# Kernel tuning notes

Hardware: AMD Instinct MI355X
Metric: run time of the kernel (lower is better)

Reference implementation:

```python
import jax, jax.numpy as jnp
import numpy as np

# Config constants (from CantorFusionConfigV2 defaults / init_kwargs)
NUM_HEADS = 8
HEAD_DIM = 64
K_NEIGHBORS = 64        # fusion_window
LEVELS = 5              # k_simplex + 1
TAU = 0.25
BASE = 3.0
ALPHA = 0.5
EPS = 1e-8
RESIDUAL_SCALE = 1.0


def _cantor_measure(S):
    """Vectorized Devil's Staircase Cantor measure for S positions in [0,1]. Returns [S]."""
    pos = (jnp.arange(S, dtype=jnp.float32) + 0.5) / S
    pos = jnp.clip(pos, 1e-10, 1.0 - 1e-10)
    ks = jnp.arange(1, LEVELS + 1, dtype=jnp.float32)
    scales = BASE ** ks                      # [L]
    lvl_w = 0.5 ** ks                        # [L]
    centers = jnp.array([0.5, 1.5, 2.5], dtype=jnp.float32)
    y = jnp.mod(pos[:, None] * scales, BASE)            # [S, L]
    logits = -((y[..., None] - centers) ** 2) / (TAU + 1e-10)  # [S, L, 3]
    p = jax.nn.softmax(logits, axis=-1)
    bits = p[..., 2] + ALPHA * p[..., 1]                # [S, L]
    return jnp.sum(bits * lvl_w, axis=-1)               # [S]


def _routes_and_weights(S):
    """KNN routes [S,K] by Cantor distance + inverse-distance softmax weights [S,K]."""
    cm = _cantor_measure(S)
    Dm = jnp.abs(cm[:, None] - cm[None, :])             # [S, S]
    Dm = Dm / (Dm.max() + 1e-10)
    neg_d, routes = jax.lax.top_k(-Dm, K_NEIGHBORS)     # k smallest distances
    route_dist = -neg_d                                  # [S, K]
    w = jax.nn.softmax(1.0 / (route_dist + EPS), axis=-1)
    return routes, w


def setup_inputs() -> dict:
    key = jax.random.key(0)
    k1, k2, k3 = jax.random.split(key, 3)
    B, S, D = 2, 2048, 512
    x = jax.random.normal(k1, (B, S, D), dtype=jnp.float32)
    W_in = jax.random.normal(k2, (D, D), dtype=jnp.float32) * (1.0 / np.sqrt(D))
    b_in = jnp.zeros((D,), dtype=jnp.float32)
    W_out = jax.random.normal(k3, (D, D), dtype=jnp.float32) * (1.0 / np.sqrt(D))
    b_out = jnp.zeros((D,), dtype=jnp.float32)
    return {"x": x, "W_in": W_in, "b_in": b_in, "W_out": W_out, "b_out": b_out}


def reference(x, W_in, b_in, W_out, b_out):
    B, S, dim = x.shape
    routes, w = _routes_and_weights(S)                   # [S,K], [S,K] (no-grad geometry)
    routes = jax.lax.stop_gradient(routes)
    w = jax.lax.stop_gradient(w)
    # input projection and head split -> [B, H, S, D]
    h = (x @ W_in + b_in).reshape(B, S, NUM_HEADS, HEAD_DIM).transpose(0, 2, 1, 3)
    # neighbor gather [B, H, S, K, D] then inverse-distance weighted sum
    gathered = h[:, :, routes, :]                        # [B,H,S,K,D]
    fused = jnp.einsum('bhskd,sk->bhsd', gathered, w)    # [B,H,S,D]
    out = fused.transpose(0, 2, 1, 3).reshape(B, S, dim) @ W_out + b_out
    return x + RESIDUAL_SCALE * out
```

## Files before the change

kernel.cpp:

```cpp
#include <hip/hip_runtime.h>
#include <hip/hip_bf16.h>

#define S_LEN 2048
#define K_NB  64

typedef __attribute__((ext_vector_type(8))) short bf16x8;
typedef __attribute__((ext_vector_type(4))) float f32x4;
typedef __attribute__((ext_vector_type(4))) unsigned int u32x4;

__device__ inline unsigned short f2b(float f) {
    unsigned u = __builtin_bit_cast(unsigned, f);
    return (unsigned short)((u + 0x7FFFu + ((u >> 16) & 1u)) >> 16);
}

__global__ __launch_bounds__(256) void prep_kernel(const float* __restrict__ W_in,
                                                   const float* __restrict__ W_out,
                                                   unsigned short* __restrict__ Wt_in,
                                                   unsigned short* __restrict__ Wt_out,
                                                   float* __restrict__ cmf) {
    int b = blockIdx.x;
    if (b < 256) {
        int t = b * 256 + threadIdx.x;
        const float* W = (t & 32768) ? W_out : W_in;
        unsigned short* Wt = (t & 32768) ? Wt_out : Wt_in;
        int u = t & 32767;
        int n = u & 511, kc = (u >> 9) * 8;
        unsigned short tmp[8];
        #pragma unroll
        for (int j = 0; j < 8; ++j) tmp[j] = f2b(W[(size_t)(kc + j) * 512 + n]);
        *(u32x4*)(Wt + (size_t)n * 512 + kc) = *(u32x4*)tmp;
    } else {
        int s = (b - 256) * 256 + threadIdx.x;
        float pos = ((float)s + 0.5f) * (1.0f / 2048.0f);
        float cm = 0.0f, scale = 1.0f, lvlw = 1.0f;
        #pragma unroll
        for (int k = 1; k <= 5; ++k) {
            scale *= 3.0f; lvlw *= 0.5f;
            float y = fmodf(pos * scale, 3.0f);
            float d0 = y - 0.5f, d1 = y - 1.5f, d2 = y - 2.5f;
            float l0 = -(d0 * d0) * 4.0f;
            float l1 = -(d1 * d1) * 4.0f;
            float l2 = -(d2 * d2) * 4.0f;
            float m = fmaxf(l0, fmaxf(l1, l2));
            float e0 = (float)exp((double)(l0 - m));
            float e1 = (float)exp((double)(l1 - m));
            float e2 = (float)exp((double)(l2 - m));
            float sum = (e0 + e1) + e2;
            float p1 = e1 / sum, p2 = e2 / sum;
            cm += (p2 + 0.5f * p1) * lvlw;
        }
        cmf[s] = cm;
    }
}

__global__ __launch_bounds__(64) void group_kernel(const float* __restrict__ cmf,
                                                   int* __restrict__ routes,
                                                   int* __restrict__ counts) {
    int s = blockIdx.x;
    int lane = threadIdx.x;
    float v = cmf[s];
    int n = 0;
    int* rt = routes + s * K_NB;
    for (int j0 = 0; j0 < S_LEN; j0 += 64) {
        float c = cmf[j0 + lane];
        bool m = (c == v);
        unsigned long long mask = __ballot(m);
        if (m) {
            int idx = n + __popcll(mask & ((1ull << lane) - 1ull));
            if (idx < K_NB) rt[idx] = j0 + lane;
        }
        n += __popcll(mask);
    }
    if (lane == 0) counts[s] = n < K_NB ? n : K_NB;
}

template <int EPI>
__global__ __launch_bounds__(256) void gemm_mfma(
    const float* __restrict__ Af, const unsigned short* __restrict__ Ab,
    const unsigned short* __restrict__ Bt, const float* __restrict__ bias,
    const float* __restrict__ X, unsigned short* __restrict__ Hb,
    float* __restrict__ Out,
    const int* __restrict__ routes, const int* __restrict__ counts) {
    __shared__ char lds[(64 + 128) * 64 * 2];
    char* As = lds;
    char* Bs = lds + 64 * 64 * 2;
    const int tid = threadIdx.x;
    const int bn = blockIdx.x, bm = blockIdx.y;
    const int wid = tid >> 6, lane = tid & 63;
    const int wr = wid >> 1, wc = wid & 1;
    const int l15 = lane & 15, l4 = lane >> 4;

    const int arow = tid >> 2;
    const int akq  = (tid & 3) * 16;
    const int brow = tid >> 1;
    const int bkh  = (tid & 1) * 32;

    auto off = [](int row, int k) -> int {
        int o = row * 128 + k * 2;
        return o ^ ((row & 7) << 4);
    };

    const int grow = bm * 64 + arow;
    const float* arow_f = nullptr;
    int gn = 1; const int* grt = nullptr; float ginv = 1.0f; size_t hbase = 0;
    if (EPI == 0) {
        arow_f = Af + (size_t)grow * 512;
    } else {
        int gs = grow & (S_LEN - 1), gb = grow >> 11;
        gn = counts[gs];
        grt = routes + gs * K_NB;
        ginv = 1.0f / (float)gn;
        hbase = (size_t)gb * S_LEN * 512;
    }
    const unsigned short* bsrc = Bt + (size_t)(bn * 128 + brow) * 512 + bkh;

    u32x4 arg[2] = {};
    u32x4 brg[4] = {};

    auto load_a = [&](int k0, u32x4* dst) {
        if (EPI == 0) {
            const float* p = arow_f + k0 + akq;
            unsigned short tmp[16];
            #pragma unroll
            for (int i = 0; i < 4; ++i) {
                float4 v = *(const float4*)(p + i * 4);
                tmp[i*4+0] = f2b(v.x); tmp[i*4+1] = f2b(v.y);
                tmp[i*4+2] = f2b(v.z); tmp[i*4+3] = f2b(v.w);
            }
            dst[0] = *(u32x4*)&tmp[0];
            dst[1] = *(u32x4*)&tmp[8];
        } else if (gn == 1) {
            const unsigned short* p = Ab + (size_t)grow * 512 + k0 + akq;
            dst[0] = *(const u32x4*)(p);
            dst[1] = *(const u32x4*)(p + 8);
        } else {
            float av[16] = {};
            for (int e = 0; e < gn; ++e) {
                const unsigned short* p = Ab + hbase + (size_t)grt[e] * 512 + k0 + akq;
                #pragma unroll
                for (int half = 0; half < 2; ++half) {
                    u32x4 u = *(const u32x4*)(p + half * 8);
                    #pragma unroll
                    for (int q = 0; q < 4; ++q) {
                        unsigned w = u[q];
                        av[half*8 + q*2 + 0] += __builtin_bit_cast(float, w << 16);
                        av[half*8 + q*2 + 1] += __builtin_bit_cast(float, w & 0xFFFF0000u);
                    }
                }
            }
            unsigned short tmp[16];
            #pragma unroll
            for (int i = 0; i < 16; ++i) tmp[i] = f2b(av[i] * ginv);
            dst[0] = *(u32x4*)&tmp[0];
            dst[1] = *(u32x4*)&tmp[8];
        }
    };
    auto load_b = [&](int k0, u32x4* dst) {
        const unsigned short* p = bsrc + k0;
        #pragma unroll
        for (int i = 0; i < 4; ++i) dst[i] = *(const u32x4*)(p + i * 8);
    };

    f32x4 acc[2][4] = {};

    load_a(0, arg);
    load_b(0, brg);
    for (int k0 = 0; k0 < 512; k0 += 64) {
        *(u32x4*)(As + off(arow, akq))     = arg[0];
        *(u32x4*)(As + off(arow, akq + 8)) = arg[1];
        #pragma unroll
        for (int i = 0; i < 4; ++i)
            *(u32x4*)(Bs + off(brow, bkh + i * 8)) = brg[i];
        __syncthreads();
        if (k0 + 64 < 512) {
            load_a(k0 + 64, arg);
            load_b(k0 + 64, brg);
        }
        #pragma unroll
        for (int kk = 0; kk < 2; ++kk) {
            const int kb = kk * 32 + l4 * 8;
            bf16x8 af[2], bg[4];
            #pragma unroll
            for (int m = 0; m < 2; ++m)
                af[m] = *(bf16x8*)(As + off(wr * 32 + m * 16 + l15, kb));
            #pragma unroll
            for (int n = 0; n < 4; ++n)
                bg[n] = *(bf16x8*)(Bs + off(wc * 64 + n * 16 + l15, kb));
            #pragma unroll
            for (int m = 0; m < 2; ++m)
                #pragma unroll
                for (int n = 0; n < 4; ++n)
                    acc[m][n] = __builtin_amdgcn_mfma_f32_16x16x32_bf16(
                        af[m], bg[n], acc[m][n], 0, 0, 0);
        }
        __syncthreads();
    }

    float bv[4];
    #pragma unroll
    for (int n = 0; n < 4; ++n) bv[n] = bias[bn * 128 + wc * 64 + n * 16 + l15];
    #pragma unroll
    for (int m = 0; m < 2; ++m) {
        #pragma unroll
        for (int r = 0; r < 4; ++r) {
            int row = bm * 64 + wr * 32 + m * 16 + l4 * 4 + r;
            #pragma unroll
            for (int n = 0; n < 4; ++n) {
                int col = bn * 128 + wc * 64 + n * 16 + l15;
                float v = acc[m][n][r] + bv[n];
                if (EPI == 0)
                    Hb[(size_t)row * 512 + col] = f2b(v);
                else
                    Out[(size_t)row * 512 + col] = X[(size_t)row * 512 + col] + v;
            }
        }
    }
}

extern "C" void kernel_launch(void* const* d_in, const int* in_sizes, int n_in,
                              void* d_out, int out_size, void* d_ws, size_t ws_size,
                              hipStream_t stream) {
    const float* x     = (const float*)d_in[0];
    const float* W_in  = (const float*)d_in[1];
    const float* b_in  = (const float*)d_in[2];
    const float* W_out = (const float*)d_in[3];
    const float* b_out = (const float*)d_in[4];
    float* out = (float*)d_out;

    char* ws = (char*)d_ws;
    float*          cmf    = (float*)ws;
    int*            counts = (int*)(ws + 8192);
    int*            routes = (int*)(ws + 16384);
    unsigned short* Wt_in  = (unsigned short*)(ws + 16384 + 524288);
    unsigned short* Wt_out = (unsigned short*)(ws + 16384 + 2 * 524288);
    unsigned short* h      = (unsigned short*)(ws + 16384 + 3 * 524288);

    prep_kernel<<<264, 256, 0, stream>>>(W_in, W_out, Wt_in, Wt_out, cmf);
    group_kernel<<<S_LEN, 64, 0, stream>>>(cmf, routes, counts);
    gemm_mfma<0><<<dim3(4, 64), 256, 0, stream>>>(x, nullptr, Wt_in, b_in,
                                                  nullptr, h, nullptr,
                                                  nullptr, nullptr);
    gemm_mfma<1><<<dim3(4, 64), 256, 0, stream>>>(nullptr, h, Wt_out, b_out,
                                                  x, nullptr, out,
                                                  routes, counts);
}
```

Measured before the change: 36.57 us.

## Fold both projections into one combined weight and gather from x directly

Because the gather-average is linear, the two projections are folded into one combined weight (W_in·W_out) and a combined bias (b_in·W_out + b_out). A small MFMA GEMM computes the combined weight, and it runs in the same launch as the grouping step. The final GEMM then gathers and averages rows of x instead of a precomputed h, which removes the full 4096x512x512 input-projection GEMM and one kernel launch. In exchange, the combined weight is rounded to bf16 and the gather now reads fp32 x rows, which changes numerics slightly.

```diff
diff --git a/kernel.cpp b/kernel.cpp
--- a/kernel.cpp
+++ b/kernel.cpp
@@ -13,24 +13,33 @@
     return (unsigned short)((u + 0x7FFFu + ((u >> 16) & 1u)) >> 16);
 }
 
-__global__ __launch_bounds__(256) void prep_kernel(const float* __restrict__ W_in,
-                                                   const float* __restrict__ W_out,
-                                                   unsigned short* __restrict__ Wt_in,
-                                                   unsigned short* __restrict__ Wt_out,
-                                                   float* __restrict__ cmf) {
-    int b = blockIdx.x;
-    if (b < 256) {
-        int t = b * 256 + threadIdx.x;
-        const float* W = (t & 32768) ? W_out : W_in;
-        unsigned short* Wt = (t & 32768) ? Wt_out : Wt_in;
-        int u = t & 32767;
+__device__ inline int swoff(int row, int k) {
+    int o = row * 128 + k * 2;
+    return o ^ ((row & 7) << 4);
+}
+
+__global__ __launch_bounds__(256) void prep_kernel(
+    const float* __restrict__ W_in, const float* __restrict__ W_out,
+    const float* __restrict__ b_in, const float* __restrict__ b_out,
+    unsigned short* __restrict__ Wb_in, unsigned short* __restrict__ Wt_out,
+    float* __restrict__ cmf, float* __restrict__ bc) {
+    int b = blockIdx.x, tid = threadIdx.x;
+    if (b < 128) {
+        int base = (b * 256 + tid) * 8;
+        float4 v0 = *(const float4*)(W_in + base);
+        float4 v1 = *(const float4*)(W_in + base + 4);
+        unsigned short t[8] = { f2b(v0.x), f2b(v0.y), f2b(v0.z), f2b(v0.w),
+                                f2b(v1.x), f2b(v1.y), f2b(v1.z), f2b(v1.w) };
+        *(u32x4*)(Wb_in + base) = *(u32x4*)t;
+    } else if (b < 256) {
+        int u = (b - 128) * 256 + tid;
         int n = u & 511, kc = (u >> 9) * 8;
-        unsigned short tmp[8];
-        #pragma unroll
-        for (int j = 0; j < 8; ++j) tmp[j] = f2b(W[(size_t)(kc + j) * 512 + n]);
-        *(u32x4*)(Wt + (size_t)n * 512 + kc) = *(u32x4*)tmp;
-    } else {
-        int s = (b - 256) * 256 + threadIdx.x;
+        unsigned short t[8];
+        #pragma unroll
+        for (int j = 0; j < 8; ++j) t[j] = f2b(W_out[(size_t)(kc + j) * 512 + n]);
+        *(u32x4*)(Wt_out + (size_t)n * 512 + kc) = *(u32x4*)t;
+    } else if (b < 264) {
+        int s = (b - 256) * 256 + tid;
         float pos = ((float)s + 0.5f) * (1.0f / 2048.0f);
         float cm = 0.0f, scale = 1.0f, lvlw = 1.0f;
         #pragma unroll
@@ -50,37 +59,106 @@
             cm += (p2 + 0.5f * p1) * lvlw;
         }
         cmf[s] = cm;
+    } else {
+        int n = (b - 264) * 256 + tid;
+        float acc = b_out[n];
+        #pragma unroll 8
+        for (int j = 0; j < 512; ++j) acc += b_in[j] * W_out[(size_t)j * 512 + n];
+        bc[n] = acc;
     }
 }
 
-__global__ __launch_bounds__(64) void group_kernel(const float* __restrict__ cmf,
-                                                   int* __restrict__ routes,
-                                                   int* __restrict__ counts) {
-    int s = blockIdx.x;
-    int lane = threadIdx.x;
-    float v = cmf[s];
-    int n = 0;
-    int* rt = routes + s * K_NB;
-    for (int j0 = 0; j0 < S_LEN; j0 += 64) {
-        float c = cmf[j0 + lane];
-        bool m = (c == v);
-        unsigned long long mask = __ballot(m);
-        if (m) {
-            int idx = n + __popcll(mask & ((1ull << lane) - 1ull));
-            if (idx < K_NB) rt[idx] = j0 + lane;
-        }
-        n += __popcll(mask);
+__global__ __launch_bounds__(256) void mid_kernel(
+    const float* __restrict__ cmf, int* __restrict__ routes,
+    int* __restrict__ counts,
+    const unsigned short* __restrict__ Wt_out,
+    const unsigned short* __restrict__ Wb_in,
+    unsigned short* __restrict__ Wct) {
+    __shared__ char lds[(64 + 128) * 64 * 2];
+    int b = blockIdx.x, tid = threadIdx.x;
+    int wid = tid >> 6, lane = tid & 63;
+    if (b < 32) {
+        char* As = lds;
+        char* Bs = lds + 64 * 64 * 2;
+        int bm = b >> 2, bn = b & 3;
+        int wr = wid >> 1, wc = wid & 1;
+        int l15 = lane & 15, l4 = lane >> 4;
+        int arow = tid >> 2, akq = (tid & 3) * 16;
+        int brow = tid >> 1, bkh = (tid & 1) * 32;
+        const unsigned short* asrc = Wt_out + (size_t)(bm * 64 + arow) * 512 + akq;
+        const unsigned short* bsrc = Wb_in + (size_t)(bn * 128 + brow) * 512 + bkh;
+        u32x4 arg[2], brg[4];
+        auto la = [&](int k0) {
+            arg[0] = *(const u32x4*)(asrc + k0);
+            arg[1] = *(const u32x4*)(asrc + k0 + 8);
+        };
+        auto lb = [&](int k0) {
+            #pragma unroll
+            for (int i = 0; i < 4; ++i) brg[i] = *(const u32x4*)(bsrc + k0 + i * 8);
+        };
+        f32x4 acc[2][4] = {};
+        la(0); lb(0);
+        for (int k0 = 0; k0 < 512; k0 += 64) {
+            *(u32x4*)(As + swoff(arow, akq))     = arg[0];
+            *(u32x4*)(As + swoff(arow, akq + 8)) = arg[1];
+            #pragma unroll
+            for (int i = 0; i < 4; ++i)
+                *(u32x4*)(Bs + swoff(brow, bkh + i * 8)) = brg[i];
+            __syncthreads();
+            if (k0 + 64 < 512) { la(k0 + 64); lb(k0 + 64); }
+            #pragma unroll
+            for (int kk = 0; kk < 2; ++kk) {
+                const int kb = kk * 32 + l4 * 8;
+                bf16x8 af[2], bg[4];
+                #pragma unroll
+                for (int m = 0; m < 2; ++m)
+                    af[m] = *(bf16x8*)(As + swoff(wr * 32 + m * 16 + l15, kb));
+                #pragma unroll
+                for (int n = 0; n < 4; ++n)
+                    bg[n] = *(bf16x8*)(Bs + swoff(wc * 64 + n * 16 + l15, kb));
+                #pragma unroll
+                for (int m = 0; m < 2; ++m)
+                    #pragma unroll
+                    for (int n = 0; n < 4; ++n)
+                        acc[m][n] = __builtin_amdgcn_mfma_f32_16x16x32_bf16(
+                            af[m], bg[n], acc[m][n], 0, 0, 0);
+            }
+            __syncthreads();
+        }
+        #pragma unroll
+        for (int m = 0; m < 2; ++m)
+            #pragma unroll
+            for (int r = 0; r < 4; ++r) {
+                int row = bm * 64 + wr * 32 + m * 16 + l4 * 4 + r;
+                #pragma unroll
+                for (int n = 0; n < 4; ++n) {
+                    int col = bn * 128 + wc * 64 + n * 16 + l15;
+                    Wct[(size_t)row * 512 + col] = f2b(acc[m][n][r]);
+                }
+            }
+    } else {
+        int s = (b - 32) * 4 + wid;
+        float v = cmf[s];
+        int n = 0;
+        int* rt = routes + s * K_NB;
+        for (int j0 = 0; j0 < S_LEN; j0 += 64) {
+            float c = cmf[j0 + lane];
+            bool m = (c == v);
+            unsigned long long mask = __ballot(m);
+            if (m) {
+                int idx = n + __popcll(mask & ((1ull << lane) - 1ull));
+                if (idx < K_NB) rt[idx] = j0 + lane;
+            }
+            n += __popcll(mask);
+        }
+        if (lane == 0) counts[s] = n < K_NB ? n : K_NB;
     }
-    if (lane == 0) counts[s] = n < K_NB ? n : K_NB;
-}
-
-template <int EPI>
-__global__ __launch_bounds__(256) void gemm_mfma(
-    const float* __restrict__ Af, const unsigned short* __restrict__ Ab,
-    const unsigned short* __restrict__ Bt, const float* __restrict__ bias,
-    const float* __restrict__ X, unsigned short* __restrict__ Hb,
-    float* __restrict__ Out,
-    const int* __restrict__ routes, const int* __restrict__ counts) {
+}
+
+__global__ __launch_bounds__(256) void gemmF_kernel(
+    const float* __restrict__ x, const unsigned short* __restrict__ Wct,
+    const float* __restrict__ bc, const int* __restrict__ routes,
+    const int* __restrict__ counts, float* __restrict__ out) {
     __shared__ char lds[(64 + 128) * 64 * 2];
     char* As = lds;
     char* Bs = lds + 64 * 64 * 2;
@@ -89,103 +167,71 @@
     const int wid = tid >> 6, lane = tid & 63;
     const int wr = wid >> 1, wc = wid & 1;
     const int l15 = lane & 15, l4 = lane >> 4;
-
-    const int arow = tid >> 2;
-    const int akq  = (tid & 3) * 16;
-    const int brow = tid >> 1;
-    const int bkh  = (tid & 1) * 32;
-
-    auto off = [](int row, int k) -> int {
-        int o = row * 128 + k * 2;
-        return o ^ ((row & 7) << 4);
-    };
+    const int arow = tid >> 2, akq = (tid & 3) * 16;
+    const int brow = tid >> 1, bkh = (tid & 1) * 32;
 
     const int grow = bm * 64 + arow;
-    const float* arow_f = nullptr;
-    int gn = 1; const int* grt = nullptr; float ginv = 1.0f; size_t hbase = 0;
-    if (EPI == 0) {
-        arow_f = Af + (size_t)grow * 512;
-    } else {
-        int gs = grow & (S_LEN - 1), gb = grow >> 11;
-        gn = counts[gs];
-        grt = routes + gs * K_NB;
-        ginv = 1.0f / (float)gn;
-        hbase = (size_t)gb * S_LEN * 512;
-    }
-    const unsigned short* bsrc = Bt + (size_t)(bn * 128 + brow) * 512 + bkh;
-
-    u32x4 arg[2] = {};
-    u32x4 brg[4] = {};
-
-    auto load_a = [&](int k0, u32x4* dst) {
-        if (EPI == 0) {
-            const float* p = arow_f + k0 + akq;
-            unsigned short tmp[16];
+    const int gs = grow & (S_LEN - 1), gb = grow >> 11;
+    const int gn = counts[gs];
+    const int* grt = routes + gs * K_NB;
+    const float ginv = 1.0f / (float)gn;
+    const float* xrow = x + (size_t)grow * 512;
+    const size_t hbase = (size_t)gb * S_LEN * 512;
+    const unsigned short* bsrc = Wct + (size_t)(bn * 128 + brow) * 512 + bkh;
+
+    u32x4 arg[2], brg[4];
+    auto load_a = [&](int k0) {
+        unsigned short tmp[16];
+        if (gn == 1) {
+            const float* p = xrow + k0 + akq;
             #pragma unroll
             for (int i = 0; i < 4; ++i) {
                 float4 v = *(const float4*)(p + i * 4);
                 tmp[i*4+0] = f2b(v.x); tmp[i*4+1] = f2b(v.y);
                 tmp[i*4+2] = f2b(v.z); tmp[i*4+3] = f2b(v.w);
             }
-            dst[0] = *(u32x4*)&tmp[0];
-            dst[1] = *(u32x4*)&tmp[8];
-        } else if (gn == 1) {
-            const unsigned short* p = Ab + (size_t)grow * 512 + k0 + akq;
-            dst[0] = *(const u32x4*)(p);
-            dst[1] = *(const u32x4*)(p + 8);
         } else {
             float av[16] = {};
             for (int e = 0; e < gn; ++e) {
-                const unsigned short* p = Ab + hbase + (size_t)grt[e] * 512 + k0 + akq;
-                #pragma unroll
-                for (int half = 0; half < 2; ++half) {
-                    u32x4 u = *(const u32x4*)(p + half * 8);
-                    #pragma unroll
-                    for (int q = 0; q < 4; ++q) {
-                        unsigned w = u[q];
-                        av[half*8 + q*2 + 0] += __builtin_bit_cast(float, w << 16);
-                        av[half*8 + q*2 + 1] += __builtin_bit_cast(float, w & 0xFFFF0000u);
-                    }
+                const float* p = x + hbase + (size_t)grt[e] * 512 + k0 + akq;
+                #pragma unroll
+                for (int i = 0; i < 4; ++i) {
+                    float4 v = *(const float4*)(p + i * 4);
+                    av[i*4+0] += v.x; av[i*4+1] += v.y;
+                    av[i*4+2] += v.z; av[i*4+3] += v.w;
                 }
             }
-            unsigned short tmp[16];
             #pragma unroll
             for (int i = 0; i < 16; ++i) tmp[i] = f2b(av[i] * ginv);
-            dst[0] = *(u32x4*)&tmp[0];
-            dst[1] = *(u32x4*)&tmp[8];
-        }
+        }
+        arg[0] = *(u32x4*)&tmp[0];
+        arg[1] = *(u32x4*)&tmp[8];
     };
-    auto load_b = [&](int k0, u32x4* dst) {
-        const unsigned short* p = bsrc + k0;
-        #pragma unroll
-        for (int i = 0; i < 4; ++i) dst[i] = *(const u32x4*)(p + i * 8);
+    auto load_b = [&](int k0) {
+        #pragma unroll
+        for (int i = 0; i < 4; ++i) brg[i] = *(const u32x4*)(bsrc + k0 + i * 8);
     };
 
     f32x4 acc[2][4] = {};
-
-    load_a(0, arg);
-    load_b(0, brg);
+    load_a(0); load_b(0);
     for (int k0 = 0; k0 < 512; k0 += 64) {
-        *(u32x4*)(As + off(arow, akq))     = arg[0];
-        *(u32x4*)(As + off(arow, akq + 8)) = arg[1];
+        *(u32x4*)(As + swoff(arow, akq))     = arg[0];
+        *(u32x4*)(As + swoff(arow, akq + 8)) = arg[1];
         #pragma unroll
         for (int i = 0; i < 4; ++i)
-            *(u32x4*)(Bs + off(brow, bkh + i * 8)) = brg[i];
+            *(u32x4*)(Bs + swoff(brow, bkh + i * 8)) = brg[i];
         __syncthreads();
-        if (k0 + 64 < 512) {
-            load_a(k0 + 64, arg);
-            load_b(k0 + 64, brg);
-        }
+        if (k0 + 64 < 512) { load_a(k0 + 64); load_b(k0 + 64); }
         #pragma unroll
         for (int kk = 0; kk < 2; ++kk) {
             const int kb = kk * 32 + l4 * 8;
             bf16x8 af[2], bg[4];
             #pragma unroll
             for (int m = 0; m < 2; ++m)
-                af[m] = *(bf16x8*)(As + off(wr * 32 + m * 16 + l15, kb));
+                af[m] = *(bf16x8*)(As + swoff(wr * 32 + m * 16 + l15, kb));
             #pragma unroll
             for (int n = 0; n < 4; ++n)
-                bg[n] = *(bf16x8*)(Bs + off(wc * 64 + n * 16 + l15, kb));
+                bg[n] = *(bf16x8*)(Bs + swoff(wc * 64 + n * 16 + l15, kb));
             #pragma unroll
             for (int m = 0; m < 2; ++m)
                 #pragma unroll
@@ -198,9 +244,9 @@
 
     float bv[4];
     #pragma unroll
-    for (int n = 0; n < 4; ++n) bv[n] = bias[bn * 128 + wc * 64 + n * 16 + l15];
+    for (int n = 0; n < 4; ++n) bv[n] = bc[bn * 128 + wc * 64 + n * 16 + l15];
     #pragma unroll
-    for (int m = 0; m < 2; ++m) {
+    for (int m = 0; m < 2; ++m)
         #pragma unroll
         for (int r = 0; r < 4; ++r) {
             int row = bm * 64 + wr * 32 + m * 16 + l4 * 4 + r;
@@ -208,13 +254,9 @@
             for (int n = 0; n < 4; ++n) {
                 int col = bn * 128 + wc * 64 + n * 16 + l15;
                 float v = acc[m][n][r] + bv[n];
-                if (EPI == 0)
-                    Hb[(size_t)row * 512 + col] = f2b(v);
-                else
-                    Out[(size_t)row * 512 + col] = X[(size_t)row * 512 + col] + v;
-            }
-        }
-    }
+                out[(size_t)row * 512 + col] = x[(size_t)row * 512 + col] + v;
+            }
+        }
 }
 
 extern "C" void kernel_launch(void* const* d_in, const int* in_sizes, int n_in,
@@ -231,16 +273,15 @@
     float*          cmf    = (float*)ws;
     int*            counts = (int*)(ws + 8192);
     int*            routes = (int*)(ws + 16384);
-    unsigned short* Wt_in  = (unsigned short*)(ws + 16384 + 524288);
+    unsigned short* Wb_in  = (unsigned short*)(ws + 16384 + 524288);
     unsigned short* Wt_out = (unsigned short*)(ws + 16384 + 2 * 524288);
-    unsigned short* h      = (unsigned short*)(ws + 16384 + 3 * 524288);
-
-    prep_kernel<<<264, 256, 0, stream>>>(W_in, W_out, Wt_in, Wt_out, cmf);
-    group_kernel<<<S_LEN, 64, 0, stream>>>(cmf, routes, counts);
-    gemm_mfma<0><<<dim3(4, 64), 256, 0, stream>>>(x, nullptr, Wt_in, b_in,
-                                                  nullptr, h, nullptr,
-                                                  nullptr, nullptr);
-    gemm_mfma<1><<<dim3(4, 64), 256, 0, stream>>>(nullptr, h, Wt_out, b_out,
-                                                  x, nullptr, out,
-                                                  routes, counts);
-}
+    unsigned short* Wct    = (unsigned short*)(ws + 16384 + 3 * 524288);
+    float*          bc     = (float*)(ws + 16384 + 4 * 524288);
+
+    prep_kernel<<<266, 256, 0, stream>>>(W_in, W_out, b_in, b_out,
+                                         Wb_in, Wt_out, cmf, bc);
+    mid_kernel<<<544, 256, 0, stream>>>(cmf, routes, counts,
+                                        Wt_out, Wb_in, Wct);
+    gemmF_kernel<<<dim3(4, 64), 256, 0, stream>>>(x, Wct, bc,
+                                                  routes, counts, out);
+}
```

Result: slower. 51.59 us (+41.1%).
